# Optimization experiments

Hardware: AMD Instinct MI355X
Metric: run time of the kernel (lower is better)

## Reference

```python
import jax, jax.numpy as jnp
import numpy as np


def setup_inputs() -> dict:
    key = jax.random.key(0)
    ks = jax.random.split(key, 8)
    B, S, D, H, E = 4, 2048, 1024, 2048, 8
    s = 0.02  # init scale
    return {
        "x": jax.random.normal(ks[0], (B, S, D), dtype=jnp.float32),
        "gate_w": jax.random.normal(ks[1], (E, D), dtype=jnp.float32) * s,
        "w1": jax.random.normal(ks[2], (E, H, D), dtype=jnp.float32) * s,
        "b1": jnp.zeros((E, H), dtype=jnp.float32),
        "w2": jax.random.normal(ks[3], (E, H, D), dtype=jnp.float32) * s,
        "b2": jnp.zeros((E, H), dtype=jnp.float32),
        "w3": jax.random.normal(ks[4], (E, D, H), dtype=jnp.float32) * s,
        "b3": jnp.zeros((E, D), dtype=jnp.float32),
        "topk": 2,
    }


def reference(x, gate_w, w1, b1, w2, b2, w3, b3, topk):
    D = x.shape[-1]
    E = gate_w.shape[0]
    xf = x.reshape(-1, D)                      # [T, D]
    T = xf.shape[0]

    logits = xf @ gate_w.T                     # [T, E]
    vals, idx = jax.lax.top_k(logits, topk)    # [T, K]
    wts = jax.nn.softmax(vals, axis=-1)        # [T, K]

    # per-token combine weight per expert (0 if expert not in top-k)
    comb = jnp.zeros((T, E), dtype=xf.dtype).at[
        jnp.arange(T)[:, None], idx
    ].add(wts)                                 # [T, E]

    out = jnp.zeros_like(xf)
    for e in range(E):  # fixed small loop over experts
        h = (xf @ w1[e].T + b1[e]) * jax.nn.silu(xf @ w2[e].T + b2[e])  # [T, H]
        y = h @ w3[e].T + b3[e]                                           # [T, D]
        out = out + comb[:, e:e + 1] * y
    return out.reshape(x.shape)
```

## Files before the change

kernel.cpp:

```cpp
#include <hip/hip_runtime.h>
#include <hip/hip_bf16.h>
#include <stdint.h>

#define T_TOK   8192
#define D_DIM   1024
#define H_DIM   2048
#define E_EXP   8
#define NP2     4096
#define BM      256
#define CAP     (2*T_TOK + E_EXP*BM)
#define MAXMB   (CAP/BM)

using f32x4 = __attribute__((ext_vector_type(4))) float;
using s16x4 = __attribute__((ext_vector_type(4))) short;
using s16x8 = __attribute__((ext_vector_type(8))) short;

__device__ __forceinline__ short bf16_of(float f) {
  union { float f; unsigned u; } v; v.f = f;
  unsigned r = v.u + 0x7FFFu + ((v.u >> 16) & 1u);
  return (short)(r >> 16);
}
__device__ __forceinline__ float f_of_bf16(short s) {
  union { unsigned u; float f; } v; v.u = ((unsigned)(unsigned short)s) << 16;
  return v.f;
}

__device__ __forceinline__ void gload16(const void* g, void* l) {
  __builtin_amdgcn_global_load_lds(
      (const __attribute__((address_space(1))) unsigned int*)g,
      (__attribute__((address_space(3))) unsigned int*)l, 16, 0, 0);
}

__global__ __launch_bounds__(256) void conv_w12(const float* __restrict__ w1,
                                                const float* __restrict__ w2,
                                                short* __restrict__ w12b) {
  int idx = blockIdx.x * 256 + threadIdx.x;
  int e = idx >> 20;
  int rem = idx & 0xFFFFF;
  int np = rem >> 8;
  int kc = rem & 255;
  int g = np >> 5, tt = np & 31, half = tt >> 4, srow = g * 16 + (tt & 15);
  const f32x4* src = (const f32x4*)(half ? w2 : w1) + ((size_t)e * H_DIM + srow) * 256 + kc;
  f32x4 v = *src;
  s16x4 o;
  o[0] = bf16_of(v[0]); o[1] = bf16_of(v[1]); o[2] = bf16_of(v[2]); o[3] = bf16_of(v[3]);
  ((s16x4*)w12b)[idx] = o;
}

__global__ __launch_bounds__(256) void conv_w3(const float* __restrict__ w3,
                                               short* __restrict__ w3b) {
  int idx = blockIdx.x * 256 + threadIdx.x;
  f32x4 v = ((const f32x4*)w3)[idx];
  s16x4 o;
  o[0] = bf16_of(v[0]); o[1] = bf16_of(v[1]); o[2] = bf16_of(v[2]); o[3] = bf16_of(v[3]);
  ((s16x4*)w3b)[idx] = o;
}

__global__ __launch_bounds__(256) void gate_kernel(const float* __restrict__ x,
                                                   const float* __restrict__ gw,
                                                   int* __restrict__ tok_e,
                                                   float* __restrict__ gatew) {
  __shared__ float g[E_EXP * D_DIM];
  int tid = threadIdx.x;
  for (int i = tid; i < E_EXP * 256; i += 256)
    ((f32x4*)g)[i] = ((const f32x4*)gw)[i];
  __syncthreads();
  int w = tid >> 6, lane = tid & 63;
  int t = blockIdx.x * 4 + w;
  float acc[E_EXP] = {};
  const f32x4* xrow = (const f32x4*)(x + (size_t)t * D_DIM);
#pragma unroll
  for (int i = 0; i < 4; ++i) {
    f32x4 xv = xrow[lane + 64 * i];
#pragma unroll
    for (int e = 0; e < E_EXP; ++e) {
      f32x4 gv = ((const f32x4*)g)[e * 256 + lane + 64 * i];
      acc[e] += xv[0] * gv[0] + xv[1] * gv[1] + xv[2] * gv[2] + xv[3] * gv[3];
    }
  }
#pragma unroll
  for (int e = 0; e < E_EXP; ++e)
#pragma unroll
    for (int off = 1; off < 64; off <<= 1)
      acc[e] += __shfl_xor(acc[e], off);
  if (lane == 0) {
    int i0 = 0; float v0 = acc[0];
    for (int e = 1; e < E_EXP; ++e) if (acc[e] > v0) { v0 = acc[e]; i0 = e; }
    int i1 = -1; float v1 = -1e30f;
    for (int e = 0; e < E_EXP; ++e) if (e != i0 && acc[e] > v1) { v1 = acc[e]; i1 = e; }
    float z = __expf(v1 - v0);
    tok_e[2 * t] = i0; tok_e[2 * t + 1] = i1;
    gatew[2 * t] = 1.f / (1.f + z); gatew[2 * t + 1] = z / (1.f + z);
  }
}

__global__ __launch_bounds__(256) void hist_kernel(const int* __restrict__ tok_e,
                                                   int* __restrict__ counts) {
  __shared__ int bc[E_EXP];
  const int tid = threadIdx.x, lane = tid & 63;
  if (tid < E_EXP) bc[tid] = 0;
  __syncthreads();
  const int4 v = ((const int4*)tok_e)[blockIdx.x * 256 + tid];
#pragma unroll
  for (int e = 0; e < E_EXP; ++e) {
    int cnt = __popcll(__ballot(v.x == e)) + __popcll(__ballot(v.y == e)) +
              __popcll(__ballot(v.z == e)) + __popcll(__ballot(v.w == e));
    if (lane == 0 && cnt) atomicAdd(&bc[e], cnt);
  }
  __syncthreads();
  if (tid < E_EXP && bc[tid]) atomicAdd(&counts[tid], bc[tid]);
}

__global__ void scan_kernel(const int* __restrict__ counts, int* __restrict__ off,
                            int* __restrict__ mb2e, int* __restrict__ mb2row) {
  if (threadIdx.x == 0 && blockIdx.x == 0) {
    int acc = 0, mb = 0;
    for (int e = 0; e < E_EXP; ++e) {
      off[e] = acc;
      int nb = (counts[e] + BM - 1) / BM;
      for (int b = 0; b < nb; ++b) { mb2e[mb] = e; mb2row[mb] = acc + b * BM; ++mb; }
      acc += nb * BM;
    }
    off[E_EXP] = acc;
    for (; mb < MAXMB; ++mb) mb2e[mb] = -1;
  }
}

__global__ __launch_bounds__(256) void assign_kernel(const int* __restrict__ tok_e,
                                                     const int* __restrict__ off,
                                                     int* __restrict__ fill,
                                                     int* __restrict__ perm,
                                                     int* __restrict__ tok_slot) {
  __shared__ int wcnt[4][E_EXP];
  __shared__ int wbase[4][E_EXP];
  const int tid = threadIdx.x, lane = tid & 63, wid = tid >> 6;
  if (tid < 32) wcnt[tid >> 3][tid & 7] = 0;
  __syncthreads();
  const int ent = blockIdx.x * 256 + tid;
  const int e = tok_e[ent];
  int myrank = 0;
#pragma unroll
  for (int e0 = 0; e0 < E_EXP; ++e0) {
    unsigned long long m = __ballot(e == e0);
    if (e == e0) {
      myrank = __popcll(m & ((1ull << lane) - 1ull));
      if (myrank == 0) wcnt[wid][e0] = __popcll(m);
    }
  }
  __syncthreads();
  if (tid < E_EXP) {
    int tot = wcnt[0][tid] + wcnt[1][tid] + wcnt[2][tid] + wcnt[3][tid];
    int base = tot ? atomicAdd(&fill[tid], tot) : 0;
#pragma unroll
    for (int w = 0; w < 4; ++w) { wbase[w][tid] = base; base += wcnt[w][tid]; }
  }
  __syncthreads();
  const int slot = off[e] + wbase[wid][e] + myrank;
  perm[slot] = ent >> 1;
  tok_slot[ent] = slot;
}

__global__ __launch_bounds__(128) void gather_kernel(const float* __restrict__ x,
                                                     const int* __restrict__ off,
                                                     const int* __restrict__ counts,
                                                     const int* __restrict__ perm,
                                                     short* __restrict__ Xp) {
  int s = blockIdx.x, tid = threadIdx.x;
  int e = -1;
#pragma unroll
  for (int i = 0; i < E_EXP; ++i)
    if (s >= off[i] && s < off[i + 1]) { e = i; break; }
  bool valid = false; int t = 0;
  if (e >= 0) { int r = s - off[e]; if (r < counts[e]) { valid = true; t = perm[s]; } }
  s16x8 o;
  if (valid) {
    const f32x4* xr = (const f32x4*)(x + (size_t)t * D_DIM);
    f32x4 a = xr[tid * 2], b = xr[tid * 2 + 1];
    o[0] = bf16_of(a[0]); o[1] = bf16_of(a[1]); o[2] = bf16_of(a[2]); o[3] = bf16_of(a[3]);
    o[4] = bf16_of(b[0]); o[5] = bf16_of(b[1]); o[6] = bf16_of(b[2]); o[7] = bf16_of(b[3]);
  } else {
#pragma unroll
    for (int j = 0; j < 8; ++j) o[j] = 0;
  }
  *(s16x8*)(Xp + (size_t)s * D_DIM + tid * 8) = o;
}

__global__ __launch_bounds__(512, 2)
void gemm12_k64(const short* __restrict__ A,
                const short* __restrict__ Bw,
                const int* __restrict__ mb2e,
                const int* __restrict__ mb2row,
                const float* __restrict__ b1v,
                const float* __restrict__ b2v,
                short* __restrict__ Out) {
  constexpr int K = D_DIM;
  constexpr int NT = K / 64;
  constexpr int BUFB = 65536;
  __shared__ alignas(16) char lds[2 * BUFB];

  const int mb = blockIdx.y;
  const int e = mb2e[mb];
  if (e < 0) return;
  const int row0 = mb2row[mb];
  const int bn = blockIdx.x;

  const int tid = threadIdx.x;
  const int lane = tid & 63;
  const int wid = tid >> 6;
  const int wr = wid >> 2, wc = wid & 3;

  const char* gA = (const char*)(A + (size_t)row0 * K);
  const char* gB = (const char*)(Bw + ((size_t)e * NP2 + (size_t)bn * 256) * K);

  auto stage_unit = [&](const char* g, int kt, int ks, char* dst) {
#pragma unroll
    for (int r = 0; r < 2; ++r) {
      const int row = r * 128 + (tid >> 2);
      const int lq = (tid & 3) ^ ((row >> 1) & 3);
      gload16(g + (size_t)row * (K * 2) + kt * 128 + ks * 64 + lq * 16,
              dst + r * 8192 + tid * 16);
    }
  };

  f32x4 acc[8][4] = {};

  stage_unit(gB, 0, 0, lds + 32768);
  stage_unit(gA, 0, 0, lds + 0);
  stage_unit(gB, 0, 1, lds + 49152);
  stage_unit(gA, 0, 1, lds + 16384);
  asm volatile("s_waitcnt vmcnt(4)" ::: "memory");
  __builtin_amdgcn_s_barrier();
  __builtin_amdgcn_sched_barrier(0);

  const int qsw = (((lane >> 4) ^ ((lane >> 1) & 3)) << 4);
  const int arow = wr * 128 + (lane & 15);
  const int brow = wc * 64 + (lane & 15);

  for (int t = 0; t < NT; ++t) {
    char* cur = lds + (t & 1) * BUFB;
    char* nxt = lds + ((t + 1) & 1) * BUFB;
    const bool more = (t + 1 < NT);
    s16x8 bv[4];
#pragma unroll
    for (int p = 0; p < 4; ++p) {
      const int ks = p >> 1, half = p & 1;
      const char* abase = cur + ks * 16384;
      s16x8 av[4];
      if (half == 0) {
        const char* bbase = cur + 32768 + ks * 16384;
#pragma unroll
        for (int f = 0; f < 4; ++f)
          bv[f] = *(const s16x8*)(bbase + (size_t)(brow + f * 16) * 64 + qsw);
      }
#pragma unroll
      for (int f = 0; f < 4; ++f)
        av[f] = *(const s16x8*)(abase + (size_t)(arow + half * 64 + f * 16) * 64 + qsw);
      if (more) {
        if (p == 0)      stage_unit(gB, t + 1, 0, nxt + 32768);
        else if (p == 1) stage_unit(gA, t + 1, 0, nxt + 0);
        else if (p == 2) stage_unit(gB, t + 1, 1, nxt + 49152);
        else             stage_unit(gA, t + 1, 1, nxt + 16384);
      }
      if (p == 1) {
        if (t == NT - 1) asm volatile("s_waitcnt vmcnt(0)" ::: "memory");
        else             asm volatile("s_waitcnt vmcnt(4)" ::: "memory");
      }
      if (p == 3 && t < NT - 1) asm volatile("s_waitcnt vmcnt(4)" ::: "memory");
      __builtin_amdgcn_s_barrier();
      asm volatile("s_waitcnt lgkmcnt(0)" ::: "memory");
      __builtin_amdgcn_sched_barrier(0);
      __builtin_amdgcn_s_setprio(1);
#pragma unroll
      for (int mf2 = 0; mf2 < 4; ++mf2)
#pragma unroll
        for (int nf = 0; nf < 4; ++nf)
          acc[half * 4 + mf2][nf] =
              __builtin_amdgcn_mfma_f32_16x16x32_bf16(av[mf2], bv[nf], acc[half * 4 + mf2][nf], 0, 0, 0);
      __builtin_amdgcn_s_setprio(0);
      __builtin_amdgcn_s_barrier();
    }
  }

#pragma unroll
  for (int mf = 0; mf < 8; ++mf) {
    const int mrow = row0 + wr * 128 + (mf >> 2) * 64 + (mf & 3) * 16 + ((lane >> 4) << 2);
#pragma unroll
    for (int p = 0; p < 2; ++p) {
      const int hcol = bn * 128 + wc * 32 + p * 16 + (lane & 15);
      const float bb1 = b1v[e * H_DIM + hcol];
      const float bb2 = b2v[e * H_DIM + hcol];
      const f32x4 a1 = acc[mf][2 * p], a2 = acc[mf][2 * p + 1];
#pragma unroll
      for (int j = 0; j < 4; ++j) {
        float x1 = a1[j] + bb1, x2 = a2[j] + bb2;
        float hv = x1 * (x2 / (1.f + __expf(-x2)));
        Out[(size_t)(mrow + j) * H_DIM + hcol] = bf16_of(hv);
      }
    }
  }
}

template <int K, int BN_, int EPI>
__global__ __launch_bounds__(512, (BN_ == 128) ? 4 : 2)
void gemm256(const short* __restrict__ A,
             const short* __restrict__ Bw,
             const int* __restrict__ mb2e,
             const int* __restrict__ mb2row,
             const float* __restrict__ biasA,
             const float* __restrict__ biasB,
             short* __restrict__ Out) {
  constexpr int NFULL = (EPI == 0) ? NP2 : D_DIM;
  constexpr int OUTLD = (EPI == 0) ? H_DIM : D_DIM;
  constexpr int KB = K * 2;
  constexpr int NT = K / 32;
  constexpr int NBF = BN_ / 64;
  constexpr int ABYTES = 16384;
  constexpr int BBYTES = BN_ * 64;
  constexpr int BUFB = ABYTES + BBYTES;
  constexpr int NB_LOADS = BN_ / 128;

  const int mb = blockIdx.y;
  const int e = mb2e[mb];
  if (e < 0) return;
  const int row0 = mb2row[mb];
  const int bn = blockIdx.x;

  __shared__ alignas(16) char lds[3 * BUFB];

  const int tid = threadIdx.x;
  const int lane = tid & 63;
  const int wid = tid >> 6;
  const int wr = wid >> 2;
  const int wc = wid & 3;

  const char* gA = (const char*)(A + (size_t)row0 * K);
  const char* gB = (const char*)(Bw + ((size_t)e * NFULL + (size_t)bn * BN_) * K);

  const int srow0 = tid >> 2, spq = tid & 3;

  f32x4 acc[8][NBF] = {};

  auto stageA = [&](int kt, int buf) {
#pragma unroll
    for (int r = 0; r < 2; ++r) {
      const int row = r * 128 + srow0;
      const int lq = spq ^ ((row >> 1) & 3);
      gload16(gA + (size_t)row * KB + kt * 64 + lq * 16,
              lds + buf * BUFB + r * 8192 + tid * 16);
    }
  };
  auto stageB = [&](int kt, int buf) {
#pragma unroll
    for (int r = 0; r < NB_LOADS; ++r) {
      const int row = r * 128 + srow0;
      const int lq = spq ^ ((row >> 1) & 3);
      gload16(gB + (size_t)row * KB + kt * 64 + lq * 16,
              lds + buf * BUFB + ABYTES + r * 8192 + tid * 16);
    }
  };

  stageA(0, 0); stageB(0, 0);
  stageA(1, 1); stageB(1, 1);
  if constexpr (BN_ == 256) asm volatile("s_waitcnt vmcnt(4)" ::: "memory");
  else                      asm volatile("s_waitcnt vmcnt(3)" ::: "memory");
  __builtin_amdgcn_s_barrier();
  __builtin_amdgcn_sched_barrier(0);

  const int qsw = (((lane >> 4) ^ ((lane >> 1) & 3)) << 4);
  const int arow = wr * 128 + (lane & 15);
  const int brow = wc * (BN_ / 4) + (lane & 15);

  int bc = 0;
  int b2 = 2;
  for (int t = 0; t < NT; ++t) {
    const char* bufb = lds + bc * BUFB;
    const char* pa = bufb + arow * 64 + qsw;
    const char* pb = bufb + ABYTES + brow * 64 + qsw;
    s16x8 av[4], bv[NBF];
#pragma unroll
    for (int f = 0; f < NBF; ++f) bv[f] = *(const s16x8*)(pb + f * 1024);
#pragma unroll
    for (int f = 0; f < 4; ++f) av[f] = *(const s16x8*)(pa + f * 1024);
    if (t + 2 < NT) stageA(t + 2, b2);
    __builtin_amdgcn_s_setprio(1);
#pragma unroll
    for (int mf = 0; mf < 4; ++mf)
#pragma unroll
      for (int nf = 0; nf < NBF; ++nf)
        acc[mf][nf] = __builtin_amdgcn_mfma_f32_16x16x32_bf16(av[mf], bv[nf], acc[mf][nf], 0, 0, 0);
    __builtin_amdgcn_s_setprio(0);
#pragma unroll
    for (int f = 0; f < 4; ++f) av[f] = *(const s16x8*)(pa + (4 + f) * 1024);
    if (t + 2 < NT) stageB(t + 2, b2);
    __builtin_amdgcn_s_setprio(1);
#pragma unroll
    for (int mf = 0; mf < 4; ++mf)
#pragma unroll
      for (int nf = 0; nf < NBF; ++nf)
        acc[4 + mf][nf] = __builtin_amdgcn_mfma_f32_16x16x32_bf16(av[mf], bv[nf], acc[4 + mf][nf], 0, 0, 0);
    __builtin_amdgcn_s_setprio(0);

    if (t < NT - 1) {
      __builtin_amdgcn_sched_barrier(0);
      if (t == NT - 2)          asm volatile("s_waitcnt vmcnt(0)" ::: "memory");
      else if (BN_ == 256)      asm volatile("s_waitcnt vmcnt(4)" ::: "memory");
      else                      asm volatile("s_waitcnt vmcnt(3)" ::: "memory");
      __builtin_amdgcn_s_barrier();
      __builtin_amdgcn_sched_barrier(0);
    }
    bc = (bc == 2) ? 0 : bc + 1;
    b2 = (b2 == 2) ? 0 : b2 + 1;
  }

  if constexpr (EPI == 0) {
#pragma unroll
    for (int mf = 0; mf < 8; ++mf) {
      const int mrow = row0 + wr * 128 + mf * 16 + ((lane >> 4) << 2);
#pragma unroll
      for (int p = 0; p < 2; ++p) {
        const int hcol = bn * 128 + wc * 32 + p * 16 + (lane & 15);
        const float bb1 = biasA[e * H_DIM + hcol];
        const float bb2 = biasB[e * H_DIM + hcol];
        const f32x4 a1 = acc[mf][2 * p], a2 = acc[mf][2 * p + 1];
#pragma unroll
        for (int j = 0; j < 4; ++j) {
          float x1 = a1[j] + bb1, x2 = a2[j] + bb2;
          float hv = x1 * (x2 / (1.f + __expf(-x2)));
          Out[(size_t)(mrow + j) * OUTLD + hcol] = bf16_of(hv);
        }
      }
    }
  } else {
#pragma unroll
    for (int mf = 0; mf < 8; ++mf) {
      const int mrow = row0 + wr * 128 + mf * 16 + ((lane >> 4) << 2);
#pragma unroll
      for (int nf = 0; nf < NBF; ++nf) {
        const int col = bn * BN_ + wc * (BN_ / 4) + nf * 16 + (lane & 15);
        const float bb = biasA[e * D_DIM + col];
#pragma unroll
        for (int j = 0; j < 4; ++j)
          Out[(size_t)(mrow + j) * OUTLD + col] = bf16_of(acc[mf][nf][j] + bb);
      }
    }
  }
}

__global__ __launch_bounds__(128) void combine_kernel(const short* __restrict__ ysb,
                                                      const int* __restrict__ tok_slot,
                                                      const float* __restrict__ gatew,
                                                      float* __restrict__ out) {
  int t = blockIdx.x, tid = threadIdx.x;
  int s0 = tok_slot[2 * t], s1 = tok_slot[2 * t + 1];
  float w0 = gatew[2 * t], w1 = gatew[2 * t + 1];
  s16x8 a = *(const s16x8*)(ysb + (size_t)s0 * D_DIM + tid * 8);
  s16x8 b = *(const s16x8*)(ysb + (size_t)s1 * D_DIM + tid * 8);
  float* op = out + (size_t)t * D_DIM + tid * 8;
  f32x4 o0, o1;
#pragma unroll
  for (int j = 0; j < 4; ++j) o0[j] = w0 * f_of_bf16(a[j]) + w1 * f_of_bf16(b[j]);
#pragma unroll
  for (int j = 0; j < 4; ++j) o1[j] = w0 * f_of_bf16(a[4 + j]) + w1 * f_of_bf16(b[4 + j]);
  *(f32x4*)op = o0;
  *(f32x4*)(op + 4) = o1;
}

extern "C" void kernel_launch(void* const* d_in, const int* in_sizes, int n_in,
                              void* d_out, int out_size, void* d_ws, size_t ws_size,
                              hipStream_t stream) {
  const float* x  = (const float*)d_in[0];
  const float* gw = (const float*)d_in[1];
  const float* w1 = (const float*)d_in[2];
  const float* b1 = (const float*)d_in[3];
  const float* w2 = (const float*)d_in[4];
  const float* b2 = (const float*)d_in[5];
  const float* w3 = (const float*)d_in[6];
  const float* b3 = (const float*)d_in[7];
  float* out = (float*)d_out;

  char* ws = (char*)d_ws;
  size_t o = 0;
  short* w12b = (short*)(ws + o); o += (size_t)E_EXP * NP2 * D_DIM * 2;
  short* w3b  = (short*)(ws + o); o += (size_t)E_EXP * D_DIM * H_DIM * 2;
  short* Xp   = (short*)(ws + o); o += (size_t)CAP * D_DIM * 2;
  short* ysb  = Xp;
  short* hbuf = (short*)(ws + o); o += (size_t)CAP * H_DIM * 2;
  int* meta     = (int*)(ws + o);
  int* counts   = meta;
  int* fill     = meta + 8;
  int* offv     = meta + 16;
  int* mb2e     = meta + 32;
  int* mb2row   = meta + 112;
  int* tok_e    = meta + 192;
  int* tok_slot = tok_e + 2 * T_TOK;
  int* perm     = tok_slot + 2 * T_TOK;
  float* gatew  = (float*)(perm + CAP);
  const size_t ws_needed = o + (192 + 4 * T_TOK + CAP + 2 * T_TOK) * sizeof(int);
  if (ws_size < ws_needed) return;

  hipMemsetAsync(counts, 0, 16 * sizeof(int), stream);

  conv_w12<<<(E_EXP * NP2 * 256) / 256, 256, 0, stream>>>(w1, w2, w12b);
  conv_w3 <<<(E_EXP * D_DIM * (H_DIM / 4)) / 256, 256, 0, stream>>>(w3, w3b);
  gate_kernel<<<T_TOK / 4, 256, 0, stream>>>(x, gw, tok_e, gatew);
  hist_kernel<<<(2 * T_TOK) / 1024, 256, 0, stream>>>(tok_e, counts);
  scan_kernel<<<1, 64, 0, stream>>>(counts, offv, mb2e, mb2row);
  assign_kernel<<<(2 * T_TOK) / 256, 256, 0, stream>>>(tok_e, offv, fill, perm, tok_slot);
  gather_kernel<<<CAP, 128, 0, stream>>>(x, offv, counts, perm, Xp);
  gemm12_k64<<<dim3(NP2 / 256, MAXMB), 512, 0, stream>>>(Xp, w12b, mb2e, mb2row, b1, b2, hbuf);
  gemm256<H_DIM, 256, 1><<<dim3(D_DIM / 256, MAXMB), 512, 0, stream>>>(hbuf, w3b, mb2e, mb2row, b3, b3, ysb);
  combine_kernel<<<T_TOK, 128, 0, stream>>>(ysb, tok_slot, gatew, out);
}
```

Baseline: 379.0 us.

## Restructure gate/up GEMM to 128-byte K rows with 8-way swizzle and fewer barriers

```diff
diff --git a/kernel.cpp b/kernel.cpp
--- a/kernel.cpp
+++ b/kernel.cpp
@@ -186,17 +186,18 @@
 }
 
 __global__ __launch_bounds__(512, 2)
-void gemm12_k64(const short* __restrict__ A,
-                const short* __restrict__ Bw,
-                const int* __restrict__ mb2e,
-                const int* __restrict__ mb2row,
-                const float* __restrict__ b1v,
-                const float* __restrict__ b2v,
-                short* __restrict__ Out) {
+void gemm12_bk64(const short* __restrict__ A,
+                 const short* __restrict__ Bw,
+                 const int* __restrict__ mb2e,
+                 const int* __restrict__ mb2row,
+                 const float* __restrict__ b1v,
+                 const float* __restrict__ b2v,
+                 short* __restrict__ Out) {
   constexpr int K = D_DIM;
+  constexpr int KB = K * 2;
   constexpr int NT = K / 64;
-  constexpr int BUFB = 65536;
-  __shared__ alignas(16) char lds[2 * BUFB];
+  constexpr int HBYTES = 32768;
+  constexpr int BUFB = 2 * HBYTES;
 
   const int mb = blockIdx.y;
   const int e = mb2e[mb];
@@ -204,86 +205,84 @@
   const int row0 = mb2row[mb];
   const int bn = blockIdx.x;
 
+  __shared__ alignas(16) char lds[2 * BUFB];
+
   const int tid = threadIdx.x;
   const int lane = tid & 63;
   const int wid = tid >> 6;
-  const int wr = wid >> 2, wc = wid & 3;
+  const int wr = wid >> 2;
+  const int wc = wid & 3;
 
   const char* gA = (const char*)(A + (size_t)row0 * K);
   const char* gB = (const char*)(Bw + ((size_t)e * NP2 + (size_t)bn * 256) * K);
 
-  auto stage_unit = [&](const char* g, int kt, int ks, char* dst) {
-#pragma unroll
-    for (int r = 0; r < 2; ++r) {
-      const int row = r * 128 + (tid >> 2);
-      const int lq = (tid & 3) ^ ((row >> 1) & 3);
-      gload16(g + (size_t)row * (K * 2) + kt * 128 + ks * 64 + lq * 16,
-              dst + r * 8192 + tid * 16);
+  f32x4 acc[8][4] = {};
+
+  auto stage = [&](int kt, int buf, int which) {
+    const char* g = which ? gB : gA;
+    char* l = lds + buf * BUFB + which * HBYTES;
+#pragma unroll
+    for (int r = 0; r < 4; ++r) {
+      const int row = r * 64 + (tid >> 3);
+      const int lq = (tid & 7) ^ (row & 7);
+      gload16(g + (size_t)row * KB + kt * 128 + lq * 16,
+              l + r * 8192 + tid * 16);
     }
   };
 
-  f32x4 acc[8][4] = {};
-
-  stage_unit(gB, 0, 0, lds + 32768);
-  stage_unit(gA, 0, 0, lds + 0);
-  stage_unit(gB, 0, 1, lds + 49152);
-  stage_unit(gA, 0, 1, lds + 16384);
-  asm volatile("s_waitcnt vmcnt(4)" ::: "memory");
+  stage(0, 0, 0); stage(0, 0, 1);
+  asm volatile("s_waitcnt vmcnt(0)" ::: "memory");
   __builtin_amdgcn_s_barrier();
   __builtin_amdgcn_sched_barrier(0);
 
-  const int qsw = (((lane >> 4) ^ ((lane >> 1) & 3)) << 4);
   const int arow = wr * 128 + (lane & 15);
   const int brow = wc * 64 + (lane & 15);
+  const int lsw = lane & 7;
 
   for (int t = 0; t < NT; ++t) {
-    char* cur = lds + (t & 1) * BUFB;
-    char* nxt = lds + ((t + 1) & 1) * BUFB;
+    const char* bufb = lds + (t & 1) * BUFB;
+    const int nb = (t + 1) & 1;
     const bool more = (t + 1 < NT);
-    s16x8 bv[4];
-#pragma unroll
-    for (int p = 0; p < 4; ++p) {
-      const int ks = p >> 1, half = p & 1;
-      const char* abase = cur + ks * 16384;
-      s16x8 av[4];
-      if (half == 0) {
-        const char* bbase = cur + 32768 + ks * 16384;
-#pragma unroll
-        for (int f = 0; f < 4; ++f)
-          bv[f] = *(const s16x8*)(bbase + (size_t)(brow + f * 16) * 64 + qsw);
-      }
+#pragma unroll
+    for (int ks = 0; ks < 2; ++ks) {
+      const int q = ((ks * 4 + (lane >> 4)) ^ lsw) * 16;
+      s16x8 av[4], bv[4];
 #pragma unroll
       for (int f = 0; f < 4; ++f)
-        av[f] = *(const s16x8*)(abase + (size_t)(arow + half * 64 + f * 16) * 64 + qsw);
-      if (more) {
-        if (p == 0)      stage_unit(gB, t + 1, 0, nxt + 32768);
-        else if (p == 1) stage_unit(gA, t + 1, 0, nxt + 0);
-        else if (p == 2) stage_unit(gB, t + 1, 1, nxt + 49152);
-        else             stage_unit(gA, t + 1, 1, nxt + 16384);
-      }
-      if (p == 1) {
-        if (t == NT - 1) asm volatile("s_waitcnt vmcnt(0)" ::: "memory");
-        else             asm volatile("s_waitcnt vmcnt(4)" ::: "memory");
-      }
-      if (p == 3 && t < NT - 1) asm volatile("s_waitcnt vmcnt(4)" ::: "memory");
+        bv[f] = *(const s16x8*)(bufb + HBYTES + (size_t)(brow + f * 16) * 128 + q);
+#pragma unroll
+      for (int f = 0; f < 4; ++f)
+        av[f] = *(const s16x8*)(bufb + (size_t)(arow + f * 16) * 128 + q);
+      if (more) stage(t + 1, nb, ks);
+      __builtin_amdgcn_s_setprio(1);
+#pragma unroll
+      for (int mf = 0; mf < 4; ++mf)
+#pragma unroll
+        for (int nf = 0; nf < 4; ++nf)
+          acc[mf][nf] = __builtin_amdgcn_mfma_f32_16x16x32_bf16(av[mf], bv[nf], acc[mf][nf], 0, 0, 0);
+      __builtin_amdgcn_s_setprio(0);
+#pragma unroll
+      for (int f = 0; f < 4; ++f)
+        av[f] = *(const s16x8*)(bufb + (size_t)(arow + 64 + f * 16) * 128 + q);
+      __builtin_amdgcn_s_setprio(1);
+#pragma unroll
+      for (int mf = 0; mf < 4; ++mf)
+#pragma unroll
+        for (int nf = 0; nf < 4; ++nf)
+          acc[4 + mf][nf] = __builtin_amdgcn_mfma_f32_16x16x32_bf16(av[mf], bv[nf], acc[4 + mf][nf], 0, 0, 0);
+      __builtin_amdgcn_s_setprio(0);
+    }
+    if (t < NT - 1) {
+      __builtin_amdgcn_sched_barrier(0);
+      asm volatile("s_waitcnt vmcnt(0)" ::: "memory");
       __builtin_amdgcn_s_barrier();
-      asm volatile("s_waitcnt lgkmcnt(0)" ::: "memory");
       __builtin_amdgcn_sched_barrier(0);
-      __builtin_amdgcn_s_setprio(1);
-#pragma unroll
-      for (int mf2 = 0; mf2 < 4; ++mf2)
-#pragma unroll
-        for (int nf = 0; nf < 4; ++nf)
-          acc[half * 4 + mf2][nf] =
-              __builtin_amdgcn_mfma_f32_16x16x32_bf16(av[mf2], bv[nf], acc[half * 4 + mf2][nf], 0, 0, 0);
-      __builtin_amdgcn_s_setprio(0);
-      __builtin_amdgcn_s_barrier();
     }
   }
 
 #pragma unroll
   for (int mf = 0; mf < 8; ++mf) {
-    const int mrow = row0 + wr * 128 + (mf >> 2) * 64 + (mf & 3) * 16 + ((lane >> 4) << 2);
+    const int mrow = row0 + wr * 128 + mf * 16 + ((lane >> 4) << 2);
 #pragma unroll
     for (int p = 0; p < 2; ++p) {
       const int hcol = bn * 128 + wc * 32 + p * 16 + (lane & 15);
@@ -300,24 +299,18 @@
   }
 }
 
-template <int K, int BN_, int EPI>
-__global__ __launch_bounds__(512, (BN_ == 128) ? 4 : 2)
-void gemm256(const short* __restrict__ A,
-             const short* __restrict__ Bw,
-             const int* __restrict__ mb2e,
-             const int* __restrict__ mb2row,
-             const float* __restrict__ biasA,
-             const float* __restrict__ biasB,
-             short* __restrict__ Out) {
-  constexpr int NFULL = (EPI == 0) ? NP2 : D_DIM;
-  constexpr int OUTLD = (EPI == 0) ? H_DIM : D_DIM;
+__global__ __launch_bounds__(512, 2)
+void gemm3_k32(const short* __restrict__ A,
+               const short* __restrict__ Bw,
+               const int* __restrict__ mb2e,
+               const int* __restrict__ mb2row,
+               const float* __restrict__ b3v,
+               short* __restrict__ Out) {
+  constexpr int K = H_DIM;
   constexpr int KB = K * 2;
   constexpr int NT = K / 32;
-  constexpr int NBF = BN_ / 64;
   constexpr int ABYTES = 16384;
-  constexpr int BBYTES = BN_ * 64;
-  constexpr int BUFB = ABYTES + BBYTES;
-  constexpr int NB_LOADS = BN_ / 128;
+  constexpr int BUFB = 2 * ABYTES;
 
   const int mb = blockIdx.y;
   const int e = mb2e[mb];
@@ -334,11 +327,11 @@
   const int wc = wid & 3;
 
   const char* gA = (const char*)(A + (size_t)row0 * K);
-  const char* gB = (const char*)(Bw + ((size_t)e * NFULL + (size_t)bn * BN_) * K);
+  const char* gB = (const char*)(Bw + ((size_t)e * D_DIM + (size_t)bn * 256) * K);
 
   const int srow0 = tid >> 2, spq = tid & 3;
 
-  f32x4 acc[8][NBF] = {};
+  f32x4 acc[8][4] = {};
 
   auto stageA = [&](int kt, int buf) {
 #pragma unroll
@@ -351,7 +344,7 @@
   };
   auto stageB = [&](int kt, int buf) {
 #pragma unroll
-    for (int r = 0; r < NB_LOADS; ++r) {
+    for (int r = 0; r < 2; ++r) {
       const int row = r * 128 + srow0;
       const int lq = spq ^ ((row >> 1) & 3);
       gload16(gB + (size_t)row * KB + kt * 64 + lq * 16,
@@ -361,14 +354,13 @@
 
   stageA(0, 0); stageB(0, 0);
   stageA(1, 1); stageB(1, 1);
-  if constexpr (BN_ == 256) asm volatile("s_waitcnt vmcnt(4)" ::: "memory");
-  else                      asm volatile("s_waitcnt vmcnt(3)" ::: "memory");
+  asm volatile("s_waitcnt vmcnt(4)" ::: "memory");
   __builtin_amdgcn_s_barrier();
   __builtin_amdgcn_sched_barrier(0);
 
   const int qsw = (((lane >> 4) ^ ((lane >> 1) & 3)) << 4);
   const int arow = wr * 128 + (lane & 15);
-  const int brow = wc * (BN_ / 4) + (lane & 15);
+  const int brow = wc * 64 + (lane & 15);
 
   int bc = 0;
   int b2 = 2;
@@ -376,9 +368,9 @@
     const char* bufb = lds + bc * BUFB;
     const char* pa = bufb + arow * 64 + qsw;
     const char* pb = bufb + ABYTES + brow * 64 + qsw;
-    s16x8 av[4], bv[NBF];
-#pragma unroll
-    for (int f = 0; f < NBF; ++f) bv[f] = *(const s16x8*)(pb + f * 1024);
+    s16x8 av[4], bv[4];
+#pragma unroll
+    for (int f = 0; f < 4; ++f) bv[f] = *(const s16x8*)(pb + f * 1024);
 #pragma unroll
     for (int f = 0; f < 4; ++f) av[f] = *(const s16x8*)(pa + f * 1024);
     if (t + 2 < NT) stageA(t + 2, b2);
@@ -386,7 +378,7 @@
 #pragma unroll
     for (int mf = 0; mf < 4; ++mf)
 #pragma unroll
-      for (int nf = 0; nf < NBF; ++nf)
+      for (int nf = 0; nf < 4; ++nf)
         acc[mf][nf] = __builtin_amdgcn_mfma_f32_16x16x32_bf16(av[mf], bv[nf], acc[mf][nf], 0, 0, 0);
     __builtin_amdgcn_s_setprio(0);
 #pragma unroll
@@ -396,15 +388,14 @@
 #pragma unroll
     for (int mf = 0; mf < 4; ++mf)
 #pragma unroll
-      for (int nf = 0; nf < NBF; ++nf)
+      for (int nf = 0; nf < 4; ++nf)
         acc[4 + mf][nf] = __builtin_amdgcn_mfma_f32_16x16x32_bf16(av[mf], bv[nf], acc[4 + mf][nf], 0, 0, 0);
     __builtin_amdgcn_s_setprio(0);
 
     if (t < NT - 1) {
       __builtin_amdgcn_sched_barrier(0);
-      if (t == NT - 2)          asm volatile("s_waitcnt vmcnt(0)" ::: "memory");
-      else if (BN_ == 256)      asm volatile("s_waitcnt vmcnt(4)" ::: "memory");
-      else                      asm volatile("s_waitcnt vmcnt(3)" ::: "memory");
+      if (t == NT - 2) asm volatile("s_waitcnt vmcnt(0)" ::: "memory");
+      else             asm volatile("s_waitcnt vmcnt(4)" ::: "memory");
       __builtin_amdgcn_s_barrier();
       __builtin_amdgcn_sched_barrier(0);
     }
@@ -412,36 +403,16 @@
     b2 = (b2 == 2) ? 0 : b2 + 1;
   }
 
-  if constexpr (EPI == 0) {
-#pragma unroll
-    for (int mf = 0; mf < 8; ++mf) {
-      const int mrow = row0 + wr * 128 + mf * 16 + ((lane >> 4) << 2);
-#pragma unroll
-      for (int p = 0; p < 2; ++p) {
-        const int hcol = bn * 128 + wc * 32 + p * 16 + (lane & 15);
-        const float bb1 = biasA[e * H_DIM + hcol];
-        const float bb2 = biasB[e * H_DIM + hcol];
-        const f32x4 a1 = acc[mf][2 * p], a2 = acc[mf][2 * p + 1];
-#pragma unroll
-        for (int j = 0; j < 4; ++j) {
-          float x1 = a1[j] + bb1, x2 = a2[j] + bb2;
-          float hv = x1 * (x2 / (1.f + __expf(-x2)));
-          Out[(size_t)(mrow + j) * OUTLD + hcol] = bf16_of(hv);
-        }
-      }
-    }
-  } else {
-#pragma unroll
-    for (int mf = 0; mf < 8; ++mf) {
-      const int mrow = row0 + wr * 128 + mf * 16 + ((lane >> 4) << 2);
-#pragma unroll
-      for (int nf = 0; nf < NBF; ++nf) {
-        const int col = bn * BN_ + wc * (BN_ / 4) + nf * 16 + (lane & 15);
-        const float bb = biasA[e * D_DIM + col];
-#pragma unroll
-        for (int j = 0; j < 4; ++j)
-          Out[(size_t)(mrow + j) * OUTLD + col] = bf16_of(acc[mf][nf][j] + bb);
-      }
+#pragma unroll
+  for (int mf = 0; mf < 8; ++mf) {
+    const int mrow = row0 + wr * 128 + mf * 16 + ((lane >> 4) << 2);
+#pragma unroll
+    for (int nf = 0; nf < 4; ++nf) {
+      const int col = bn * 256 + wc * 64 + nf * 16 + (lane & 15);
+      const float bb = b3v[e * D_DIM + col];
+#pragma unroll
+      for (int j = 0; j < 4; ++j)
+        Out[(size_t)(mrow + j) * D_DIM + col] = bf16_of(acc[mf][nf][j] + bb);
     }
   }
 }
@@ -507,7 +478,7 @@
   scan_kernel<<<1, 64, 0, stream>>>(counts, offv, mb2e, mb2row);
   assign_kernel<<<(2 * T_TOK) / 256, 256, 0, stream>>>(tok_e, offv, fill, perm, tok_slot);
   gather_kernel<<<CAP, 128, 0, stream>>>(x, offv, counts, perm, Xp);
-  gemm12_k64<<<dim3(NP2 / 256, MAXMB), 512, 0, stream>>>(Xp, w12b, mb2e, mb2row, b1, b2, hbuf);
-  gemm256<H_DIM, 256, 1><<<dim3(D_DIM / 256, MAXMB), 512, 0, stream>>>(hbuf, w3b, mb2e, mb2row, b3, b3, ysb);
+  gemm12_bk64<<<dim3(NP2 / 256, MAXMB), 512, 0, stream>>>(Xp, w12b, mb2e, mb2row, b1, b2, hbuf);
+  gemm3_k32<<<dim3(D_DIM / 256, MAXMB), 512, 0, stream>>>(hbuf, w3b, mb2e, mb2row, b3, ysb);
   combine_kernel<<<T_TOK, 128, 0, stream>>>(ysb, tok_slot, gatew, out);
 }
```

After: 380.0 us. No clear change (+0.3%).
